# Kernel optimization log

Measured on AMD Instinct MI355X. Metric: run time of the kernel, lower is better.

The kernel has to match this reference:

```python
import jax, jax.numpy as jnp
import numpy as np

EPS = 1e-8
N, D, H, O0, O1, R = 512, 64, 64, 32, 32, 16


def _norm_eps(x, axis, keepdims=False):
    # regularized norm: sqrt(clamp(sum(x^2), min=EPS))
    return jnp.sqrt(jnp.maximum(jnp.sum(x * x, axis=axis, keepdims=keepdims), EPS))


def _radial(x, w1, b1, w2, b2):
    # tiny 2-layer MLP: relu(x@w1+b1)@w2+b2
    return jax.nn.relu(x @ w1 + b1) @ w2 + b2


def _filter1(x, rij, w1, b1, w2, b2):
    rad = _radial(x, w1, b1, w2, b2)            # [N,N,out]
    dij = jnp.linalg.norm(rij, axis=-1)          # [N,N]
    rad = jnp.where((dij < EPS)[..., None], jnp.zeros_like(rad), rad)
    u = rij / _norm_eps(rij, -1, keepdims=True)  # unit vectors [N,N,3]
    # [N,N,1,3] * [N,N,out,1] -> [N,N,out,3]
    return u[..., None, :] * rad[..., None]


def _mlp_params(key, din, dh, dout, prefix):
    k1, k2, k3, k4 = jax.random.split(key, 4)
    s1 = 1.0 / np.sqrt(din)
    s2 = 1.0 / np.sqrt(dh)
    return {
        prefix + '_w1': jax.random.uniform(k1, (din, dh), jnp.float32, -s1, s1),
        prefix + '_b1': jax.random.uniform(k2, (dh,), jnp.float32, -s1, s1),
        prefix + '_w2': jax.random.uniform(k3, (dh, dout), jnp.float32, -s2, s2),
        prefix + '_b2': jax.random.uniform(k4, (dout,), jnp.float32, -s2, s2),
    }


def setup_inputs() -> dict:
    key = jax.random.key(0)
    ks = jax.random.split(key, 7)
    inp = {
        'x0': jax.random.normal(ks[0], (N, N, D), jnp.float32),
        'x1': jax.random.normal(ks[1], (N, N, D), jnp.float32),
        'rbf': jax.random.normal(ks[2], (N, N, R), jnp.float32),
        'rij': jax.random.normal(ks[3], (N, N, 3), jnp.float32),
    }
    inp.update(_mlp_params(ks[4], D, H, O0, 'f0'))
    inp.update(_mlp_params(ks[5], D, H, O0, 'f10'))
    inp.update(_mlp_params(ks[6], D, H, O1, 'f11'))
    return inp


def reference(x0, x1, rbf, rij,
              f0_w1, f0_b1, f0_w2, f0_b2,
              f10_w1, f10_b1, f10_w2, f10_b2,
              f11_w1, f11_b1, f11_w2, f11_b2):
    # output list m=0: filter0 applied to x0 (key 0) then x1 (key 1)
    out0_a = _radial(x0, f0_w1, f0_b1, f0_w2, f0_b2)[..., None]   # [N,N,O0,1]
    out0_b = _radial(x1, f0_w1, f0_b1, f0_w2, f0_b2)[..., None]   # [N,N,O0,1]
    # output list m=1: filter1_to_1(x0), filter1_to_0(x1), filter1_to_1(x1)
    out1_a = _filter1(x0, rij, f11_w1, f11_b1, f11_w2, f11_b2)    # [N,N,O1,3]
    out1_b = _filter1(x1, rij, f10_w1, f10_b1, f10_w2, f10_b2)    # [N,N,O0,3]
    out1_c = _filter1(x1, rij, f11_w1, f11_b1, f11_w2, f11_b2)    # [N,N,O1,3]
    return (out0_a, out0_b, out1_a, out1_b, out1_c)
```

## Files before the change

kernel.cpp:

```cpp
#include <hip/hip_runtime.h>

#define NN 512
#define NP (NN*NN)

typedef __bf16 bf16x8 __attribute__((ext_vector_type(8)));
typedef float  f32x4  __attribute__((ext_vector_type(4)));


__global__ __launch_bounds__(256) void conv_fused_kernel(
    const float* __restrict__ x0, const float* __restrict__ x1,
    const float* __restrict__ rij,
    const float* __restrict__ w1_0, const float* __restrict__ b1_0,
    const float* __restrict__ w2_0, const float* __restrict__ b2_0,
    const float* __restrict__ w1_1, const float* __restrict__ b1_1,
    const float* __restrict__ w2_1, const float* __restrict__ b2_1,
    const float* __restrict__ w1_2, const float* __restrict__ b1_2,
    const float* __restrict__ w2_2, const float* __restrict__ b2_2,
    float* __restrict__ out)
{
    __shared__ __attribute__((aligned(16))) __bf16 sW1T[3][64][72];
    __shared__ __attribute__((aligned(16))) __bf16 sW2T[3][32][72];
    __shared__ float sB1[3][64];
    __shared__ float sB2[3][32];
    __shared__ __attribute__((aligned(16))) __bf16 sH[4][16][72];
    __shared__ float sU[4][16][4];

    const int tid = threadIdx.x;
    const int wv  = tid >> 6;
    const int ln  = tid & 63;
    const int l16 = ln & 15;
    const int q   = ln >> 4;

    {
        const float* w1s[3] = {w1_0, w1_1, w1_2};
        const float* w2s[3] = {w2_0, w2_1, w2_2};
        const float* b1s[3] = {b1_0, b1_1, b1_2};
        const float* b2s[3] = {b2_0, b2_1, b2_2};
        for (int w = 0; w < 3; ++w) {
            for (int e = tid; e < 64*64; e += 256) {
                int k = e >> 6, n = e & 63;
                sW1T[w][n][k] = (__bf16)w1s[w][e];
            }
            for (int e = tid; e < 64*32; e += 256) {
                int k = e >> 5, n = e & 31;
                sW2T[w][n][k] = (__bf16)w2s[w][e];
            }
            if (tid < 64) sB1[w][tid] = b1s[w][tid];
            if (tid < 32) sB2[w][tid] = b2s[w][tid];
        }
    }
    __syncthreads();

    const size_t OB0a = 0;
    const size_t OB0b = (size_t)NP * 32;
    const size_t OB1a = (size_t)NP * 64;
    const size_t OB1b = OB1a + (size_t)NP * 96;
    const size_t OB1c = OB1b + (size_t)NP * 96;

    const int xsel[5]    = {0, 1, 0, 1, 1};
    const int wsel[5]    = {0, 0, 2, 1, 2};
    const size_t obase[5] = {OB0a, OB0b, OB1a, OB1b, OB1c};

    for (int t = 0; t < 4; ++t) {
        const int p0 = blockIdx.x * 256 + (t * 4 + wv) * 16;

        if (ln < 16) {
            const float* rp = rij + (size_t)(p0 + ln) * 3;
            float r0 = rp[0], r1 = rp[1], r2 = rp[2];
            float s  = r0*r0 + r1*r1 + r2*r2;
            float inv = (s < 1e-16f) ? 0.0f : (1.0f / sqrtf(fmaxf(s, 1e-8f)));
            sU[wv][ln][0] = r0 * inv;
            sU[wv][ln][1] = r1 * inv;
            sU[wv][ln][2] = r2 * inv;
        }

        bf16x8 ax[2][2];
        {
            const float* xs[2] = {x0, x1};
            #pragma unroll
            for (int xi = 0; xi < 2; ++xi) {
                const float* xr = xs[xi] + (size_t)(p0 + l16) * 64 + q * 8;
                #pragma unroll
                for (int ks = 0; ks < 2; ++ks) {
                    float4 v0 = *(const float4*)(xr + ks * 32);
                    float4 v1 = *(const float4*)(xr + ks * 32 + 4);
                    bf16x8 a;
                    a[0] = (__bf16)v0.x; a[1] = (__bf16)v0.y;
                    a[2] = (__bf16)v0.z; a[3] = (__bf16)v0.w;
                    a[4] = (__bf16)v1.x; a[5] = (__bf16)v1.y;
                    a[6] = (__bf16)v1.z; a[7] = (__bf16)v1.w;
                    ax[xi][ks] = a;
                }
            }
        }

        asm volatile("s_waitcnt lgkmcnt(0)" ::: "memory");

        for (int rd = 0; rd < 5; ++rd) {
            const int w = wsel[rd];

            f32x4 acc[4];
            #pragma unroll
            for (int nt = 0; nt < 4; ++nt) acc[nt] = (f32x4){0.f, 0.f, 0.f, 0.f};
            #pragma unroll
            for (int nt = 0; nt < 4; ++nt) {
                #pragma unroll
                for (int ks = 0; ks < 2; ++ks) {
                    bf16x8 b = *(const bf16x8*)&sW1T[w][nt * 16 + l16][ks * 32 + q * 8];
                    acc[nt] = __builtin_amdgcn_mfma_f32_16x16x32_bf16(
                        ax[xsel[rd]][ks], b, acc[nt], 0, 0, 0);
                }
            }
            #pragma unroll
            for (int nt = 0; nt < 4; ++nt) {
                float bb = sB1[w][nt * 16 + l16];
                #pragma unroll
                for (int r = 0; r < 4; ++r) {
                    float h = fmaxf(acc[nt][r] + bb, 0.0f);
                    sH[wv][q * 4 + r][nt * 16 + l16] = (__bf16)h;
                }
            }
            asm volatile("s_waitcnt lgkmcnt(0)" ::: "memory");

            bf16x8 h2[2];
            h2[0] = *(const bf16x8*)&sH[wv][l16][q * 8];
            h2[1] = *(const bf16x8*)&sH[wv][l16][32 + q * 8];

            f32x4 acc2[2];
            acc2[0] = (f32x4){0.f, 0.f, 0.f, 0.f};
            acc2[1] = (f32x4){0.f, 0.f, 0.f, 0.f};
            #pragma unroll
            for (int nt = 0; nt < 2; ++nt) {
                #pragma unroll
                for (int ks = 0; ks < 2; ++ks) {
                    bf16x8 b = *(const bf16x8*)&sW2T[w][nt * 16 + l16][ks * 32 + q * 8];
                    acc2[nt] = __builtin_amdgcn_mfma_f32_16x16x32_bf16(
                        h2[ks], b, acc2[nt], 0, 0, 0);
                }
            }

            if (rd < 2) {
                #pragma unroll
                for (int nt = 0; nt < 2; ++nt) {
                    float bb = sB2[w][nt * 16 + l16];
                    #pragma unroll
                    for (int r = 0; r < 4; ++r) {
                        int p = p0 + q * 4 + r;
                        out[obase[rd] + (size_t)p * 32 + nt * 16 + l16] = acc2[nt][r] + bb;
                    }
                }
            } else {
                #pragma unroll
                for (int nt = 0; nt < 2; ++nt) {
                    float bb = sB2[w][nt * 16 + l16];
                    #pragma unroll
                    for (int r = 0; r < 4; ++r) {
                        int pr = q * 4 + r;
                        int p  = p0 + pr;
                        float rv = acc2[nt][r] + bb;
                        size_t base = obase[rd] + ((size_t)p * 32 + nt * 16 + l16) * 3;
                        out[base + 0] = rv * sU[wv][pr][0];
                        out[base + 1] = rv * sU[wv][pr][1];
                        out[base + 2] = rv * sU[wv][pr][2];
                    }
                }
            }
        }
    }
}

extern "C" void kernel_launch(void* const* d_in, const int* in_sizes, int n_in,
                              void* d_out, int out_size, void* d_ws, size_t ws_size,
                              hipStream_t stream) {
    const float* x0   = (const float*)d_in[0];
    const float* x1   = (const float*)d_in[1];
    const float* rij  = (const float*)d_in[3];

    conv_fused_kernel<<<NP / 256, 256, 0, stream>>>(
        x0, x1, rij,
        (const float*)d_in[4],  (const float*)d_in[5],  (const float*)d_in[6],  (const float*)d_in[7],
        (const float*)d_in[8],  (const float*)d_in[9],  (const float*)d_in[10], (const float*)d_in[11],
        (const float*)d_in[12], (const float*)d_in[13], (const float*)d_in[14], (const float*)d_in[15],
        (float*)d_out);
}
```

Before: 516.9 us.

## Assign one filter per wave with register-resident weights and vectorized stores

The kernel is restructured so each of five waves handles one of the five outputs for the same 16 points. Weights and biases are kept in registers instead of shared memory. The MFMA operands are swapped so results come out point-major, which allows float4 vectorized output stores. The hidden-layer transpose now goes through ds_bpermute rather than a shared-memory round trip. This removes the shared-memory staging and the scattered scalar stores, but each wave loads its x and rij separately, so input reads are duplicated across waves and register pressure goes up.

```diff
diff --git a/kernel.cpp b/kernel.cpp
--- a/kernel.cpp
+++ b/kernel.cpp
@@ -2,12 +2,19 @@
 
 #define NN 512
 #define NP (NN*NN)
+#define TILES 8
+
 
 typedef __bf16 bf16x8 __attribute__((ext_vector_type(8)));
 typedef float  f32x4  __attribute__((ext_vector_type(4)));
 
-
-__global__ __launch_bounds__(256) void conv_fused_kernel(
+static __device__ __forceinline__ unsigned pk2(float a, float b) {
+    unsigned short ua = __builtin_bit_cast(unsigned short, (__bf16)a);
+    unsigned short ub = __builtin_bit_cast(unsigned short, (__bf16)b);
+    return (unsigned)ua | ((unsigned)ub << 16);
+}
+
+__global__ __launch_bounds__(320, 2) void conv_fused_kernel(
     const float* __restrict__ x0, const float* __restrict__ x1,
     const float* __restrict__ rij,
     const float* __restrict__ w1_0, const float* __restrict__ b1_0,
@@ -18,152 +25,161 @@
     const float* __restrict__ w2_2, const float* __restrict__ b2_2,
     float* __restrict__ out)
 {
-    __shared__ __attribute__((aligned(16))) __bf16 sW1T[3][64][72];
-    __shared__ __attribute__((aligned(16))) __bf16 sW2T[3][32][72];
-    __shared__ float sB1[3][64];
-    __shared__ float sB2[3][32];
-    __shared__ __attribute__((aligned(16))) __bf16 sH[4][16][72];
-    __shared__ float sU[4][16][4];
-
     const int tid = threadIdx.x;
     const int wv  = tid >> 6;
     const int ln  = tid & 63;
     const int l16 = ln & 15;
     const int q   = ln >> 4;
 
-    {
-        const float* w1s[3] = {w1_0, w1_1, w1_2};
-        const float* w2s[3] = {w2_0, w2_1, w2_2};
-        const float* b1s[3] = {b1_0, b1_1, b1_2};
-        const float* b2s[3] = {b2_0, b2_1, b2_2};
-        for (int w = 0; w < 3; ++w) {
-            for (int e = tid; e < 64*64; e += 256) {
-                int k = e >> 6, n = e & 63;
-                sW1T[w][n][k] = (__bf16)w1s[w][e];
+    const float* xp  = (wv == 0 || wv == 2) ? x0 : x1;
+    const int w = (wv == 3) ? 1 : ((wv >= 2) ? 2 : 0);
+    const float* w1p = (w == 0) ? w1_0 : ((w == 1) ? w1_1 : w1_2);
+    const float* w2p = (w == 0) ? w2_0 : ((w == 1) ? w2_1 : w2_2);
+    const float* b1p = (w == 0) ? b1_0 : ((w == 1) ? b1_1 : b1_2);
+    const float* b2p = (w == 0) ? b2_0 : ((w == 1) ? b2_1 : b2_2);
+    const size_t obase =
+        (wv == 0) ? (size_t)0        :
+        (wv == 1) ? (size_t)NP *  32 :
+        (wv == 2) ? (size_t)NP *  64 :
+        (wv == 3) ? (size_t)NP * 160 :
+                    (size_t)NP * 256;
+    const bool vecout = (wv >= 2);
+
+    bf16x8 w1f[4][2];
+    #pragma unroll
+    for (int nt = 0; nt < 4; ++nt) {
+        #pragma unroll
+        for (int ks = 0; ks < 2; ++ks) {
+            bf16x8 f;
+            #pragma unroll
+            for (int j = 0; j < 8; ++j)
+                f[j] = (__bf16)w1p[(ks*32 + q*8 + j)*64 + nt*16 + l16];
+            w1f[nt][ks] = f;
+        }
+    }
+    bf16x8 w2f[2][2];
+    #pragma unroll
+    for (int nt = 0; nt < 2; ++nt) {
+        #pragma unroll
+        for (int ks = 0; ks < 2; ++ks) {
+            bf16x8 f;
+            #pragma unroll
+            for (int j = 0; j < 8; ++j)
+                f[j] = (__bf16)w2p[(ks*32 + q*8 + j)*32 + nt*16 + l16];
+            w2f[nt][ks] = f;
+        }
+    }
+    float b1r[4][4], b2r[2][4];
+    #pragma unroll
+    for (int nt = 0; nt < 4; ++nt)
+        #pragma unroll
+        for (int r = 0; r < 4; ++r) b1r[nt][r] = b1p[nt*16 + q*4 + r];
+    #pragma unroll
+    for (int nt = 0; nt < 2; ++nt)
+        #pragma unroll
+        for (int r = 0; r < 4; ++r) b2r[nt][r] = b2p[nt*16 + q*4 + r];
+
+    const int addrA = ((q & 1) * 32 + l16) * 4;
+    const int addrB = addrA + 64;
+    const bool hiq = (q >= 2);
+
+    for (int t = 0; t < TILES; ++t) {
+        const int p0 = blockIdx.x * (16 * TILES) + t * 16;
+        const int p  = p0 + l16;
+
+        bf16x8 ax[2];
+        {
+            const float* xr = xp + (size_t)p * 64 + q * 8;
+            #pragma unroll
+            for (int ks = 0; ks < 2; ++ks) {
+                float4 v0 = *(const float4*)(xr + ks * 32);
+                float4 v1 = *(const float4*)(xr + ks * 32 + 4);
+                bf16x8 a;
+                a[0]=(__bf16)v0.x; a[1]=(__bf16)v0.y; a[2]=(__bf16)v0.z; a[3]=(__bf16)v0.w;
+                a[4]=(__bf16)v1.x; a[5]=(__bf16)v1.y; a[6]=(__bf16)v1.z; a[7]=(__bf16)v1.w;
+                ax[ks] = a;
             }
-            for (int e = tid; e < 64*32; e += 256) {
-                int k = e >> 5, n = e & 31;
-                sW2T[w][n][k] = (__bf16)w2s[w][e];
-            }
-            if (tid < 64) sB1[w][tid] = b1s[w][tid];
-            if (tid < 32) sB2[w][tid] = b2s[w][tid];
-        }
-    }
-    __syncthreads();
-
-    const size_t OB0a = 0;
-    const size_t OB0b = (size_t)NP * 32;
-    const size_t OB1a = (size_t)NP * 64;
-    const size_t OB1b = OB1a + (size_t)NP * 96;
-    const size_t OB1c = OB1b + (size_t)NP * 96;
-
-    const int xsel[5]    = {0, 1, 0, 1, 1};
-    const int wsel[5]    = {0, 0, 2, 1, 2};
-    const size_t obase[5] = {OB0a, OB0b, OB1a, OB1b, OB1c};
-
-    for (int t = 0; t < 4; ++t) {
-        const int p0 = blockIdx.x * 256 + (t * 4 + wv) * 16;
-
-        if (ln < 16) {
-            const float* rp = rij + (size_t)(p0 + ln) * 3;
+        }
+
+        float u0 = 0.f, u1 = 0.f, u2 = 0.f;
+        if (vecout) {
+            const float* rp = rij + (size_t)p * 3;
             float r0 = rp[0], r1 = rp[1], r2 = rp[2];
             float s  = r0*r0 + r1*r1 + r2*r2;
             float inv = (s < 1e-16f) ? 0.0f : (1.0f / sqrtf(fmaxf(s, 1e-8f)));
-            sU[wv][ln][0] = r0 * inv;
-            sU[wv][ln][1] = r1 * inv;
-            sU[wv][ln][2] = r2 * inv;
-        }
-
-        bf16x8 ax[2][2];
-        {
-            const float* xs[2] = {x0, x1};
-            #pragma unroll
-            for (int xi = 0; xi < 2; ++xi) {
-                const float* xr = xs[xi] + (size_t)(p0 + l16) * 64 + q * 8;
+            u0 = r0 * inv; u1 = r1 * inv; u2 = r2 * inv;
+        }
+
+        f32x4 acc1[4];
+        #pragma unroll
+        for (int nt = 0; nt < 4; ++nt) acc1[nt] = (f32x4){0.f, 0.f, 0.f, 0.f};
+        #pragma unroll
+        for (int nt = 0; nt < 4; ++nt) {
+            #pragma unroll
+            for (int ks = 0; ks < 2; ++ks)
+                acc1[nt] = __builtin_amdgcn_mfma_f32_16x16x32_bf16(
+                    w1f[nt][ks], ax[ks], acc1[nt], 0, 0, 0);
+        }
+
+        unsigned dw01[4], dw23[4];
+        #pragma unroll
+        for (int nt = 0; nt < 4; ++nt) {
+            float h0 = fmaxf(acc1[nt][0] + b1r[nt][0], 0.f);
+            float h1 = fmaxf(acc1[nt][1] + b1r[nt][1], 0.f);
+            float h2 = fmaxf(acc1[nt][2] + b1r[nt][2], 0.f);
+            float h3 = fmaxf(acc1[nt][3] + b1r[nt][3], 0.f);
+            dw01[nt] = pk2(h0, h1);
+            dw23[nt] = pk2(h2, h3);
+        }
+
+        f32x4 acc2[2];
+        acc2[0] = (f32x4){0.f, 0.f, 0.f, 0.f};
+        acc2[1] = (f32x4){0.f, 0.f, 0.f, 0.f};
+        #pragma unroll
+        for (int ks = 0; ks < 2; ++ks) {
+            const int n0 = ks*2, n1 = ks*2 + 1;
+            int d0a = __builtin_amdgcn_ds_bpermute(addrA, (int)dw01[n0]);
+            int d0b = __builtin_amdgcn_ds_bpermute(addrA, (int)dw01[n1]);
+            int d1a = __builtin_amdgcn_ds_bpermute(addrA, (int)dw23[n0]);
+            int d1b = __builtin_amdgcn_ds_bpermute(addrA, (int)dw23[n1]);
+            int d2a = __builtin_amdgcn_ds_bpermute(addrB, (int)dw01[n0]);
+            int d2b = __builtin_amdgcn_ds_bpermute(addrB, (int)dw01[n1]);
+            int d3a = __builtin_amdgcn_ds_bpermute(addrB, (int)dw23[n0]);
+            int d3b = __builtin_amdgcn_ds_bpermute(addrB, (int)dw23[n1]);
+            int4 dv;
+            dv.x = hiq ? d0b : d0a;
+            dv.y = hiq ? d1b : d1a;
+            dv.z = hiq ? d2b : d2a;
+            dv.w = hiq ? d3b : d3a;
+            bf16x8 pf = __builtin_bit_cast(bf16x8, dv);
+            #pragma unroll
+            for (int nt = 0; nt < 2; ++nt)
+                acc2[nt] = __builtin_amdgcn_mfma_f32_16x16x32_bf16(
+                    w2f[nt][ks], pf, acc2[nt], 0, 0, 0);
+        }
+
+        if (!vecout) {
+            #pragma unroll
+            for (int nt = 0; nt < 2; ++nt) {
+                f32x4 v;
                 #pragma unroll
-                for (int ks = 0; ks < 2; ++ks) {
-                    float4 v0 = *(const float4*)(xr + ks * 32);
-                    float4 v1 = *(const float4*)(xr + ks * 32 + 4);
-                    bf16x8 a;
-                    a[0] = (__bf16)v0.x; a[1] = (__bf16)v0.y;
-                    a[2] = (__bf16)v0.z; a[3] = (__bf16)v0.w;
-                    a[4] = (__bf16)v1.x; a[5] = (__bf16)v1.y;
-                    a[6] = (__bf16)v1.z; a[7] = (__bf16)v1.w;
-                    ax[xi][ks] = a;
-                }
+                for (int r = 0; r < 4; ++r) v[r] = acc2[nt][r] + b2r[nt][r];
+                *(f32x4*)(out + obase + (size_t)p * 32 + nt*16 + q*4) = v;
             }
-        }
-
-        asm volatile("s_waitcnt lgkmcnt(0)" ::: "memory");
-
-        for (int rd = 0; rd < 5; ++rd) {
-            const int w = wsel[rd];
-
-            f32x4 acc[4];
-            #pragma unroll
-            for (int nt = 0; nt < 4; ++nt) acc[nt] = (f32x4){0.f, 0.f, 0.f, 0.f};
-            #pragma unroll
-            for (int nt = 0; nt < 4; ++nt) {
-                #pragma unroll
-                for (int ks = 0; ks < 2; ++ks) {
-                    bf16x8 b = *(const bf16x8*)&sW1T[w][nt * 16 + l16][ks * 32 + q * 8];
-                    acc[nt] = __builtin_amdgcn_mfma_f32_16x16x32_bf16(
-                        ax[xsel[rd]][ks], b, acc[nt], 0, 0, 0);
-                }
-            }
-            #pragma unroll
-            for (int nt = 0; nt < 4; ++nt) {
-                float bb = sB1[w][nt * 16 + l16];
-                #pragma unroll
-                for (int r = 0; r < 4; ++r) {
-                    float h = fmaxf(acc[nt][r] + bb, 0.0f);
-                    sH[wv][q * 4 + r][nt * 16 + l16] = (__bf16)h;
-                }
-            }
-            asm volatile("s_waitcnt lgkmcnt(0)" ::: "memory");
-
-            bf16x8 h2[2];
-            h2[0] = *(const bf16x8*)&sH[wv][l16][q * 8];
-            h2[1] = *(const bf16x8*)&sH[wv][l16][32 + q * 8];
-
-            f32x4 acc2[2];
-            acc2[0] = (f32x4){0.f, 0.f, 0.f, 0.f};
-            acc2[1] = (f32x4){0.f, 0.f, 0.f, 0.f};
+        } else {
             #pragma unroll
             for (int nt = 0; nt < 2; ++nt) {
-                #pragma unroll
-                for (int ks = 0; ks < 2; ++ks) {
-                    bf16x8 b = *(const bf16x8*)&sW2T[w][nt * 16 + l16][ks * 32 + q * 8];
-                    acc2[nt] = __builtin_amdgcn_mfma_f32_16x16x32_bf16(
-                        h2[ks], b, acc2[nt], 0, 0, 0);
-                }
-            }
-
-            if (rd < 2) {
-                #pragma unroll
-                for (int nt = 0; nt < 2; ++nt) {
-                    float bb = sB2[w][nt * 16 + l16];
-                    #pragma unroll
-                    for (int r = 0; r < 4; ++r) {
-                        int p = p0 + q * 4 + r;
-                        out[obase[rd] + (size_t)p * 32 + nt * 16 + l16] = acc2[nt][r] + bb;
-                    }
-                }
-            } else {
-                #pragma unroll
-                for (int nt = 0; nt < 2; ++nt) {
-                    float bb = sB2[w][nt * 16 + l16];
-                    #pragma unroll
-                    for (int r = 0; r < 4; ++r) {
-                        int pr = q * 4 + r;
-                        int p  = p0 + pr;
-                        float rv = acc2[nt][r] + bb;
-                        size_t base = obase[rd] + ((size_t)p * 32 + nt * 16 + l16) * 3;
-                        out[base + 0] = rv * sU[wv][pr][0];
-                        out[base + 1] = rv * sU[wv][pr][1];
-                        out[base + 2] = rv * sU[wv][pr][2];
-                    }
-                }
+                float rv0 = acc2[nt][0] + b2r[nt][0];
+                float rv1 = acc2[nt][1] + b2r[nt][1];
+                float rv2 = acc2[nt][2] + b2r[nt][2];
+                float rv3 = acc2[nt][3] + b2r[nt][3];
+                f32x4 va = {rv0*u0, rv0*u1, rv0*u2, rv1*u0};
+                f32x4 vb = {rv1*u1, rv1*u2, rv2*u0, rv2*u1};
+                f32x4 vc = {rv2*u2, rv3*u0, rv3*u1, rv3*u2};
+                float* op = out + obase + ((size_t)p * 32 + nt*16 + q*4) * 3;
+                *(f32x4*)(op + 0) = va;
+                *(f32x4*)(op + 4) = vb;
+                *(f32x4*)(op + 8) = vc;
             }
         }
     }
@@ -176,7 +192,7 @@
     const float* x1   = (const float*)d_in[1];
     const float* rij  = (const float*)d_in[3];
 
-    conv_fused_kernel<<<NP / 256, 256, 0, stream>>>(
+    conv_fused_kernel<<<NP / (16 * TILES), 320, 0, stream>>>(
         x0, x1, rij,
         (const float*)d_in[4],  (const float*)d_in[5],  (const float*)d_in[6],  (const float*)d_in[7],
         (const float*)d_in[8],  (const float*)d_in[9],  (const float*)d_in[10], (const float*)d_in[11],
```

Measured after the change: 556.0 us. 7.6% more time.
